# Performance work log

Hardware: AMD Instinct MI355X
Metric: run time of the kernel (lower is better)

The kernel has to match this reference:

```python
import jax, jax.numpy as jnp
import numpy as np

N_HEAD = 16

def setup_inputs() -> dict:
    key = jax.random.key(0)
    k1, k2, k3 = jax.random.split(key, 3)
    B, S, D = 4, 2048, 1024
    x = jax.random.normal(k1, (B, S, D), dtype=jnp.float32)
    w_attn = jax.random.normal(k2, (D, 3 * D), dtype=jnp.float32) * 0.02
    b_attn = jnp.zeros((3 * D,), dtype=jnp.float32)
    w_proj = jax.random.normal(k3, (D, D), dtype=jnp.float32) * 0.02
    b_proj = jnp.zeros((D,), dtype=jnp.float32)
    return {"x": x, "w_attn": w_attn, "b_attn": b_attn, "w_proj": w_proj, "b_proj": b_proj}

def reference(x, w_attn, b_attn, w_proj, b_proj):
    B, S, D = x.shape
    H = N_HEAD
    dh = D // H
    # c_attn (fan_in_fan_out Conv1D-style: y = x @ W + b)
    qkv = x @ w_attn + b_attn                      # [B,S,3D]
    q, k, v = jnp.split(qkv, 3, axis=-1)
    q = q.reshape(B, S, H, dh).transpose(0, 2, 1, 3)   # [B,H,S,dh]
    k = k.reshape(B, S, H, dh).transpose(0, 2, 3, 1)   # [B,H,dh,S]  (split_heads k=True)
    v = v.reshape(B, S, H, dh).transpose(0, 2, 1, 3)   # [B,H,S,dh]
    # scores = Q K^T, scaled by sqrt(d_head) since scale=True
    w = jnp.einsum('bhid,bhdj->bhij', q, k) / jnp.sqrt(jnp.asarray(dh, x.dtype))
    # causal mask blending exactly as original: w*b - 1e10*(1-b)
    b = jnp.tril(jnp.ones((S, S), dtype=x.dtype))[None, None]
    w = w * b - 1e10 * (1.0 - b)
    w = jax.nn.softmax(w, axis=-1)
    a = jnp.einsum('bhij,bhjd->bhid', w, v)        # [B,H,S,dh]
    a = a.transpose(0, 2, 1, 3).reshape(B, S, D)   # merge_heads
    out = a @ w_proj + b_proj                      # c_proj
    present = jnp.stack((k.transpose(0, 1, 3, 2), v))  # [2,B,H,S,dh]
    return out, present
```

## Files before the change

kernel.cpp:

```cpp
#include <hip/hip_runtime.h>
#include <stdint.h>

typedef unsigned short u16;
typedef __attribute__((ext_vector_type(8))) __bf16 bf16x8;
typedef __attribute__((ext_vector_type(4))) __bf16 bf16x4v;
typedef __attribute__((ext_vector_type(4))) float f32x4;
typedef __attribute__((ext_vector_type(4))) unsigned short u16x4;
typedef __attribute__((ext_vector_type(8))) unsigned short u16x8;

#define MFMA16(a,b,c) __builtin_amdgcn_mfma_f32_16x16x32_bf16(a,b,c,0,0,0)

static __device__ __forceinline__ float fexp2(float x){
#if __has_builtin(__builtin_amdgcn_exp2f)
  return __builtin_amdgcn_exp2f(x);
#else
  float r; asm("v_exp_f32 %0, %1" : "=v"(r) : "v"(x)); return r;
#endif
}

static __device__ __forceinline__ u16 f2b(float f){
  uint32_t u = __float_as_uint(f);
  u += 0x7fffu + ((u >> 16) & 1u);
  return (u16)(u >> 16);
}

static __device__ __forceinline__ void gload_lds16(const void* g, void* l){
  __builtin_amdgcn_global_load_lds(
      (__attribute__((address_space(1))) void*)(uintptr_t)g,
      (__attribute__((address_space(3))) void*)(uintptr_t)l,
      16, 0, 0);
}

__global__ __launch_bounds__(256) void fused_prep(
    const float* __restrict__ x, const float* __restrict__ w_attn,
    const float* __restrict__ w_proj,
    u16* __restrict__ x_bf, u16* __restrict__ wA_T, u16* __restrict__ wP_T)
{
  const int bid = blockIdx.x;
  const int tid = threadIdx.x;
  if (bid < 2048){
    const int n = 4 * 2048 * 1024;
    const int stride = 2048 * 256 * 4;
    int i = (bid * 256 + tid) * 4;
#pragma unroll
    for (int k = 0; k < 4; ++k, i += stride){
      if (i < n){
        float4 v = *(const float4*)(x + i);
        u16x4 o;
        o.x = f2b(v.x); o.y = f2b(v.y); o.z = f2b(v.z); o.w = f2b(v.w);
        *(u16x4*)(x_bf + i) = o;
      }
    }
    return;
  }
  __shared__ float tile[32][33];
  const float* in;
  u16* out;
  int K, N, nb, kb;
  if (bid < 5120){
    const int idx = bid - 2048;
    in = w_attn; out = wA_T; K = 1024; N = 3072;
    nb = (idx % 96) * 32; kb = (idx / 96) * 32;
  } else {
    const int idx = bid - 5120;
    in = w_proj; out = wP_T; K = 1024; N = 1024;
    nb = (idx % 32) * 32; kb = (idx / 32) * 32;
  }
  const int tx = tid & 31, ty = tid >> 5;
#pragma unroll
  for (int i = 0; i < 32; i += 8)
    tile[ty + i][tx] = in[(size_t)(kb + ty + i) * N + nb + tx];
  __syncthreads();
#pragma unroll
  for (int i = 0; i < 32; i += 8)
    out[(size_t)(nb + ty + i) * K + kb + tx] = f2b(tile[tx][ty + i]);
}

template<int MODE>
__global__ __launch_bounds__(512, 2) void gemm_pipe(
    const u16* __restrict__ A, const u16* __restrict__ Bt,
    const float* __restrict__ bias, float* __restrict__ Cout,
    u16* __restrict__ q_bf, u16* __restrict__ k_bf, u16* __restrict__ vT_bf,
    int N, int K)
{
  extern __shared__ u16 smem[];
  const int nT = K >> 5;
  const int tid = threadIdx.x;
  const int w = tid >> 6, lane = tid & 63;
  const int l15 = lane & 15, lhi = lane >> 4;
  const int wr = w >> 1, wc = w & 1;
  const int mBase = blockIdx.y * 256, nBase = blockIdx.x * 128;

  const int r0 = tid >> 2;
  const int ch = (tid & 3) ^ ((r0 >> 1) & 3);
  const u16* Ag  = A  + (size_t)(mBase + r0) * K + ch * 8;
  const u16* Ag2 = Ag + (size_t)128 * K;
  const u16* Bg  = Bt + (size_t)(nBase + r0) * K + ch * 8;

  f32x4 acc[4][4];
#pragma unroll
  for (int i = 0; i < 4; ++i)
#pragma unroll
    for (int j = 0; j < 4; ++j) acc[i][j] = f32x4{0.f, 0.f, 0.f, 0.f};

  auto stage = [&](int kt){
    char* buf = (char*)smem + (kt % 3) * 24576;
    const int kb = kt << 5;
    gload_lds16(Ag  + kb, buf + tid * 16);
    gload_lds16(Ag2 + kb, buf + 8192 + tid * 16);
    gload_lds16(Bg  + kb, buf + 16384 + tid * 16);
  };

  stage(0); stage(1);

  for (int kt = 0; kt < nT; ++kt){
    if (kt == nT - 1) asm volatile("s_waitcnt vmcnt(0)" ::: "memory");
    else              asm volatile("s_waitcnt vmcnt(3)" ::: "memory");
    __builtin_amdgcn_s_barrier();
    if (kt + 2 < nT) stage(kt + 2);
    const char* Ab = (const char*)smem + (kt % 3) * 24576;
    const char* Bb = Ab + 16384;
#define LDT(base, row) (*(const bf16x8*)((base) + ((row) << 6) + ((lhi ^ (((row) >> 1) & 3)) << 4)))
    bf16x8 a0, a1, a2, a3, b0, b1, b2, b3;
    {
      const int ar = wr * 64 + l15;
      a0 = LDT(Ab, ar); a1 = LDT(Ab, ar + 16); a2 = LDT(Ab, ar + 32); a3 = LDT(Ab, ar + 48);
      const int br = wc * 64 + l15;
      b0 = LDT(Bb, br); b1 = LDT(Bb, br + 16); b2 = LDT(Bb, br + 32); b3 = LDT(Bb, br + 48);
    }
#undef LDT
    __builtin_amdgcn_s_setprio(1);
    acc[0][0] = MFMA16(a0, b0, acc[0][0]); acc[0][1] = MFMA16(a0, b1, acc[0][1]);
    acc[0][2] = MFMA16(a0, b2, acc[0][2]); acc[0][3] = MFMA16(a0, b3, acc[0][3]);
    acc[1][0] = MFMA16(a1, b0, acc[1][0]); acc[1][1] = MFMA16(a1, b1, acc[1][1]);
    acc[1][2] = MFMA16(a1, b2, acc[1][2]); acc[1][3] = MFMA16(a1, b3, acc[1][3]);
    acc[2][0] = MFMA16(a2, b0, acc[2][0]); acc[2][1] = MFMA16(a2, b1, acc[2][1]);
    acc[2][2] = MFMA16(a2, b2, acc[2][2]); acc[2][3] = MFMA16(a2, b3, acc[2][3]);
    acc[3][0] = MFMA16(a3, b0, acc[3][0]); acc[3][1] = MFMA16(a3, b1, acc[3][1]);
    acc[3][2] = MFMA16(a3, b2, acc[3][2]); acc[3][3] = MFMA16(a3, b3, acc[3][3]);
    __builtin_amdgcn_s_setprio(0);
  }

  if (MODE == 0){
#pragma unroll
    for (int ni = 0; ni < 4; ++ni){
      const int col = nBase + wc * 64 + ni * 16 + l15;
      const float bv = bias[col];
#pragma unroll
      for (int mi = 0; mi < 4; ++mi)
#pragma unroll
        for (int r = 0; r < 4; ++r){
          const int row = mBase + wr * 64 + mi * 16 + lhi * 4 + r;
          Cout[(size_t)row * N + col] = acc[mi][ni][r] + bv;
        }
    }
    return;
  }

  const int sec = nBase >> 10;
  const int nn0 = nBase & 1023;
  const int bb_ = mBase >> 11;
  const int s0  = mBase & 2047;

  if (sec == 2){
#pragma unroll
    for (int ni = 0; ni < 4; ++ni){
      const int c = wc * 64 + ni * 16 + l15;
      const int nn = nn0 + c;
      const int h = nn >> 6, d = nn & 63;
      const float bv = bias[nBase + c];
#pragma unroll
      for (int mi = 0; mi < 4; ++mi){
        const int sb = s0 + wr * 64 + mi * 16 + lhi * 4;
        u16x4 pk;
#pragma unroll
        for (int r = 0; r < 4; ++r){
          const float v = acc[mi][ni][r] + bv;
          pk[r] = f2b(v);
          Cout[16777216 + ((size_t)(bb_ * 16 + h) * 2048 + sb + r) * 64 + d] = v;
        }
        *(u16x4*)(vT_bf + ((size_t)(bb_ * 16 + h) * 64 + d) * 2048 + sb) = pk;
      }
    }
    return;
  }

  __syncthreads();
  const float qscl = (sec == 0) ? 0.1803368801111204f : 1.0f;
#pragma unroll
  for (int ni = 0; ni < 4; ++ni){
    const int c = wc * 64 + ni * 16 + l15;
    const float bv = bias[nBase + c];
#pragma unroll
    for (int mi = 0; mi < 4; ++mi)
#pragma unroll
      for (int r = 0; r < 4; ++r){
        const int rl = wr * 64 + mi * 16 + lhi * 4 + r;
        smem[rl * 128 + (c ^ ((rl & 7) << 3))] = f2b((acc[mi][ni][r] + bv) * qscl);
      }
  }
  if (sec == 1){
#pragma unroll
    for (int ni = 0; ni < 4; ++ni){
      const int c = wc * 64 + ni * 16 + l15;
      const int nn = nn0 + c;
      const int h = nn >> 6, d = nn & 63;
      const float bv = bias[nBase + c];
#pragma unroll
      for (int mi = 0; mi < 4; ++mi)
#pragma unroll
        for (int r = 0; r < 4; ++r){
          const int s = s0 + wr * 64 + mi * 16 + lhi * 4 + r;
          Cout[8388608 + ((size_t)(bb_ * 16 + h) * 2048 + s) * 64 + d] = acc[mi][ni][r] + bv;
        }
    }
  }
  __syncthreads();
  {
    const int row = tid >> 1, half = tid & 1;
    u16* base = (sec == 0 ? q_bf : k_bf);
#pragma unroll
    for (int i = 0; i < 8; ++i){
      const int c0 = half * 64 + i * 8;
      const int h = (nn0 >> 6) + (c0 >> 6);
      u16x8 vv = *(const u16x8*)&smem[row * 128 + (c0 ^ ((row & 7) << 3))];
      *(u16x8*)(base + ((size_t)(bb_ * 16 + h) * 2048 + s0 + row) * 64 + (c0 & 63)) = vv;
    }
  }
}

__global__ __launch_bounds__(256) void attn_kern(
    const u16* __restrict__ q_bf, const u16* __restrict__ k_bf,
    const u16* __restrict__ vT_bf, u16* __restrict__ a_bf)
{
  const int S = 2048;
  const int id = (int)blockIdx.x + 32 * (int)blockIdx.y;
  const int xcd = id & 7, j = id >> 3;
  const int bh = xcd + 8 * (j & 7);
  const int qt = 31 - (j >> 3);

  const int tid = threadIdx.x, w = tid >> 6, lane = tid & 63;
  const int l15 = lane & 15, lhi = lane >> 4;
  const u16* qp = q_bf + (size_t)bh * S * 64;
  const char* kbytes = (const char*)(k_bf + (size_t)bh * S * 64);
  const char* vbytes = (const char*)(vT_bf + (size_t)bh * 64 * S);
  const int b = bh >> 4, h = bh & 15;

  __shared__ u16 Kbuf[2][64 * 64];
  __shared__ u16 Vbuf[2][64 * 64];
  __shared__ u16 P_all[4][16 * 64];
  char* Pc = (char*)&P_all[w][0];
  const int swz = (l15 & 7) << 4;

  const int srow = tid >> 3;
  const int sch  = (tid & 7) ^ (srow & 7);

  const int qr0 = qt * 64 + w * 16;
  const int nStage = qt + 1;

  bf16x8 qf0 = *(const bf16x8*)&qp[(qr0 + l15) * 64 + lhi * 8];
  bf16x8 qf1 = *(const bf16x8*)&qp[(qr0 + l15) * 64 + 32 + lhi * 8];

  f32x4 o[4];
#pragma unroll
  for (int df = 0; df < 4; ++df) o[df] = f32x4{0.f,0.f,0.f,0.f};
  float lsum = 0.f;

  int cur = 0;
  gload_lds16(kbytes + (size_t)srow * 128 + sch * 16,        (char*)Kbuf[0] + w * 1024);
  gload_lds16(kbytes + (size_t)(srow + 32) * 128 + sch * 16, (char*)Kbuf[0] + 4096 + w * 1024);
  gload_lds16(vbytes + (size_t)srow * 4096 + sch * 16,        (char*)Vbuf[0] + w * 1024);
  gload_lds16(vbytes + (size_t)(srow + 32) * 4096 + sch * 16, (char*)Vbuf[0] + 4096 + w * 1024);
  __syncthreads();

  for (int it = 0; it < nStage; ++it){
    const int jb = it * 64;
    if (it + 1 < nStage){
      const char* kb2 = kbytes + (size_t)(jb + 64) * 128;
      const char* vb2 = vbytes + (size_t)(jb + 64) * 2;
      char* kd = (char*)Kbuf[cur ^ 1];
      char* vd = (char*)Vbuf[cur ^ 1];
      gload_lds16(kb2 + (size_t)srow * 128 + sch * 16,        kd + w * 1024);
      gload_lds16(kb2 + (size_t)(srow + 32) * 128 + sch * 16, kd + 4096 + w * 1024);
      gload_lds16(vb2 + (size_t)srow * 4096 + sch * 16,        vd + w * 1024);
      gload_lds16(vb2 + (size_t)(srow + 32) * 4096 + sch * 16, vd + 4096 + w * 1024);
    }
    {
      const char* Kc = (const char*)Kbuf[cur];
      const char* Vc = (const char*)Vbuf[cur];
      f32x4 s[4];
      __builtin_amdgcn_s_setprio(1);
#pragma unroll
      for (int nf = 0; nf < 4; ++nf){
        const bf16x8 kf0 = *(const bf16x8*)(Kc + (((nf * 16 + l15) * 128 + 0 * 64 + lhi * 16) ^ swz));
        const bf16x8 kf1 = *(const bf16x8*)(Kc + (((nf * 16 + l15) * 128 + 1 * 64 + lhi * 16) ^ swz));
        f32x4 z = {0.f, 0.f, 0.f, 0.f};
        z = MFMA16(kf0, qf0, z);
        z = MFMA16(kf1, qf1, z);
        s[nf] = z;
      }
      __builtin_amdgcn_s_setprio(0);
      bf16x8 vf[8];
#pragma unroll
      for (int kk = 0; kk < 2; ++kk)
#pragma unroll
        for (int df = 0; df < 4; ++df)
          vf[kk*4+df] = *(const bf16x8*)(Vc + (((df * 16 + l15) * 128 + kk * 64 + lhi * 16) ^ swz));
      if (it == nStage - 1){
        const int q = qr0 + l15;
#pragma unroll
        for (int nf = 0; nf < 4; ++nf)
#pragma unroll
          for (int r = 0; r < 4; ++r){
            const int kv = jb + nf * 16 + lhi * 4 + r;
            if (kv > q) s[nf][r] = -1e10f;
          }
      }
      float p[16];
#pragma unroll
      for (int nf = 0; nf < 4; ++nf)
#pragma unroll
        for (int r = 0; r < 4; ++r) p[nf*4+r] = fexp2(s[nf][r]);
      lsum += (((p[0]+p[1])+(p[2]+p[3])) + ((p[4]+p[5])+(p[6]+p[7])))
            + (((p[8]+p[9])+(p[10]+p[11])) + ((p[12]+p[13])+(p[14]+p[15])));
#pragma unroll
      for (int nf = 0; nf < 4; ++nf){
        bf16x4v pk;
#pragma unroll
        for (int r = 0; r < 4; ++r) pk[r] = (__bf16)p[nf*4+r];
        *(bf16x4v*)(Pc + ((l15 * 128 + nf * 32 + lhi * 8) ^ swz)) = pk;
      }
      __builtin_amdgcn_s_setprio(1);
#pragma unroll
      for (int kk = 0; kk < 2; ++kk){
        const bf16x8 pa = *(const bf16x8*)(Pc + ((l15 * 128 + kk * 64 + lhi * 16) ^ swz));
#pragma unroll
        for (int df = 0; df < 4; ++df)
          o[df] = MFMA16(pa, vf[kk*4+df], o[df]);
      }
      __builtin_amdgcn_s_setprio(0);
    }
    __syncthreads();
    cur ^= 1;
  }

  {
    float rs = lsum;
    rs += __shfl_xor(rs, 16);
    rs += __shfl_xor(rs, 32);
    const float linv = 1.0f / rs;
    float lr[4];
#pragma unroll
    for (int r = 0; r < 4; ++r)
      lr[r] = __shfl(linv, (lane & 48) | (lhi * 4 + r));
#pragma unroll
    for (int r = 0; r < 4; ++r){
      const int qrow = qr0 + lhi * 4 + r;
#pragma unroll
      for (int df = 0; df < 4; ++df)
        a_bf[((size_t)b * 2048 + qrow) * 1024 + h * 64 + df * 16 + l15] = f2b(o[df][r] * lr[r]);
    }
  }
}

extern "C" void kernel_launch(void* const* d_in, const int* in_sizes, int n_in,
                              void* d_out, int out_size, void* d_ws, size_t ws_size,
                              hipStream_t stream)
{
  const float* x      = (const float*)d_in[0];
  const float* w_attn = (const float*)d_in[1];
  const float* b_attn = (const float*)d_in[2];
  const float* w_proj = (const float*)d_in[3];
  const float* b_proj = (const float*)d_in[4];
  float* out = (float*)d_out;
  char* ws = (char*)d_ws;
  const size_t MB = 1u << 20;
  u16* x_bf  = (u16*)(ws + 0);
  u16* wA_T  = (u16*)(ws + 16 * MB);
  u16* wP_T  = (u16*)(ws + 22 * MB);
  u16* q_bf  = (u16*)(ws + 24 * MB);
  u16* k_bf  = (u16*)(ws + 40 * MB);
  u16* vT_bf = (u16*)(ws + 56 * MB);
  u16* a_bf  = x_bf;

  fused_prep<<<dim3(6144), dim3(256), 0, stream>>>(x, w_attn, w_proj, x_bf, wA_T, wP_T);
  gemm_pipe<1><<<dim3(24, 32), dim3(512), 73728, stream>>>(
      x_bf, wA_T, b_attn, out, q_bf, k_bf, vT_bf, 3072, 1024);
  attn_kern<<<dim3(32, 64), dim3(256), 0, stream>>>(q_bf, k_bf, vT_bf, a_bf);
  gemm_pipe<0><<<dim3(8, 32), dim3(512), 73728, stream>>>(
      a_bf, wP_T, b_proj, out, nullptr, nullptr, nullptr, 1024, 1024);
}
```

Before: 172.7 us.

## Halve GEMM block to 4 waves, each computing 128x64 tile

```diff
diff --git a/kernel.cpp b/kernel.cpp
--- a/kernel.cpp
+++ b/kernel.cpp
@@ -77,7 +77,7 @@
 }
 
 template<int MODE>
-__global__ __launch_bounds__(512, 2) void gemm_pipe(
+__global__ __launch_bounds__(256, 2) void gemm_pipe(
     const u16* __restrict__ A, const u16* __restrict__ Bt,
     const float* __restrict__ bias, float* __restrict__ Cout,
     u16* __restrict__ q_bf, u16* __restrict__ k_bf, u16* __restrict__ vT_bf,
@@ -91,44 +91,48 @@
   const int wr = w >> 1, wc = w & 1;
   const int mBase = blockIdx.y * 256, nBase = blockIdx.x * 128;
 
-  const int r0 = tid >> 2;
-  const int ch = (tid & 3) ^ ((r0 >> 1) & 3);
-  const u16* Ag  = A  + (size_t)(mBase + r0) * K + ch * 8;
-  const u16* Ag2 = Ag + (size_t)128 * K;
-  const u16* Bg  = Bt + (size_t)(nBase + r0) * K + ch * 8;
-
-  f32x4 acc[4][4];
-#pragma unroll
-  for (int i = 0; i < 4; ++i)
+  const int qrow = lane >> 2;
+  const int ch = (lane & 3) ^ ((qrow >> 1) & 3);
+  const u16* AgB = A  + (size_t)(mBase + qrow) * K + ch * 8;
+  const u16* BgB = Bt + (size_t)(nBase + qrow) * K + ch * 8;
+  const int ln16 = lane << 4;
+
+  f32x4 acc[8][4];
+#pragma unroll
+  for (int i = 0; i < 8; ++i)
 #pragma unroll
     for (int j = 0; j < 4; ++j) acc[i][j] = f32x4{0.f, 0.f, 0.f, 0.f};
 
   auto stage = [&](int kt){
     char* buf = (char*)smem + (kt % 3) * 24576;
     const int kb = kt << 5;
-    gload_lds16(Ag  + kb, buf + tid * 16);
-    gload_lds16(Ag2 + kb, buf + 8192 + tid * 16);
-    gload_lds16(Bg  + kb, buf + 16384 + tid * 16);
+#pragma unroll
+    for (int i = 0; i < 4; ++i)
+      gload_lds16(AgB + (size_t)((w * 4 + i) * 16) * K + kb,
+                  buf + (w * 4 + i) * 1024 + ln16);
+#pragma unroll
+    for (int j = 0; j < 2; ++j)
+      gload_lds16(BgB + (size_t)((w * 2 + j) * 16) * K + kb,
+                  buf + 16384 + (w * 2 + j) * 1024 + ln16);
   };
 
   stage(0); stage(1);
 
   for (int kt = 0; kt < nT; ++kt){
     if (kt == nT - 1) asm volatile("s_waitcnt vmcnt(0)" ::: "memory");
-    else              asm volatile("s_waitcnt vmcnt(3)" ::: "memory");
+    else              asm volatile("s_waitcnt vmcnt(6)" ::: "memory");
     __builtin_amdgcn_s_barrier();
     if (kt + 2 < nT) stage(kt + 2);
     const char* Ab = (const char*)smem + (kt % 3) * 24576;
     const char* Bb = Ab + 16384;
 #define LDT(base, row) (*(const bf16x8*)((base) + ((row) << 6) + ((lhi ^ (((row) >> 1) & 3)) << 4)))
-    bf16x8 a0, a1, a2, a3, b0, b1, b2, b3;
+    bf16x8 b0, b1, b2, b3, a0, a1, a2, a3;
     {
-      const int ar = wr * 64 + l15;
-      a0 = LDT(Ab, ar); a1 = LDT(Ab, ar + 16); a2 = LDT(Ab, ar + 32); a3 = LDT(Ab, ar + 48);
       const int br = wc * 64 + l15;
       b0 = LDT(Bb, br); b1 = LDT(Bb, br + 16); b2 = LDT(Bb, br + 32); b3 = LDT(Bb, br + 48);
-    }
-#undef LDT
+      const int ar = wr * 128 + l15;
+      a0 = LDT(Ab, ar); a1 = LDT(Ab, ar + 16); a2 = LDT(Ab, ar + 32); a3 = LDT(Ab, ar + 48);
+    }
     __builtin_amdgcn_s_setprio(1);
     acc[0][0] = MFMA16(a0, b0, acc[0][0]); acc[0][1] = MFMA16(a0, b1, acc[0][1]);
     acc[0][2] = MFMA16(a0, b2, acc[0][2]); acc[0][3] = MFMA16(a0, b3, acc[0][3]);
@@ -139,6 +143,21 @@
     acc[3][0] = MFMA16(a3, b0, acc[3][0]); acc[3][1] = MFMA16(a3, b1, acc[3][1]);
     acc[3][2] = MFMA16(a3, b2, acc[3][2]); acc[3][3] = MFMA16(a3, b3, acc[3][3]);
     __builtin_amdgcn_s_setprio(0);
+    {
+      const int ar = wr * 128 + 64 + l15;
+      a0 = LDT(Ab, ar); a1 = LDT(Ab, ar + 16); a2 = LDT(Ab, ar + 32); a3 = LDT(Ab, ar + 48);
+    }
+#undef LDT
+    __builtin_amdgcn_s_setprio(1);
+    acc[4][0] = MFMA16(a0, b0, acc[4][0]); acc[4][1] = MFMA16(a0, b1, acc[4][1]);
+    acc[4][2] = MFMA16(a0, b2, acc[4][2]); acc[4][3] = MFMA16(a0, b3, acc[4][3]);
+    acc[5][0] = MFMA16(a1, b0, acc[5][0]); acc[5][1] = MFMA16(a1, b1, acc[5][1]);
+    acc[5][2] = MFMA16(a1, b2, acc[5][2]); acc[5][3] = MFMA16(a1, b3, acc[5][3]);
+    acc[6][0] = MFMA16(a2, b0, acc[6][0]); acc[6][1] = MFMA16(a2, b1, acc[6][1]);
+    acc[6][2] = MFMA16(a2, b2, acc[6][2]); acc[6][3] = MFMA16(a2, b3, acc[6][3]);
+    acc[7][0] = MFMA16(a3, b0, acc[7][0]); acc[7][1] = MFMA16(a3, b1, acc[7][1]);
+    acc[7][2] = MFMA16(a3, b2, acc[7][2]); acc[7][3] = MFMA16(a3, b3, acc[7][3]);
+    __builtin_amdgcn_s_setprio(0);
   }
 
   if (MODE == 0){
@@ -147,10 +166,10 @@
       const int col = nBase + wc * 64 + ni * 16 + l15;
       const float bv = bias[col];
 #pragma unroll
-      for (int mi = 0; mi < 4; ++mi)
+      for (int mi = 0; mi < 8; ++mi)
 #pragma unroll
         for (int r = 0; r < 4; ++r){
-          const int row = mBase + wr * 64 + mi * 16 + lhi * 4 + r;
+          const int row = mBase + wr * 128 + mi * 16 + lhi * 4 + r;
           Cout[(size_t)row * N + col] = acc[mi][ni][r] + bv;
         }
     }
@@ -170,8 +189,8 @@
       const int h = nn >> 6, d = nn & 63;
       const float bv = bias[nBase + c];
 #pragma unroll
-      for (int mi = 0; mi < 4; ++mi){
-        const int sb = s0 + wr * 64 + mi * 16 + lhi * 4;
+      for (int mi = 0; mi < 8; ++mi){
+        const int sb = s0 + wr * 128 + mi * 16 + lhi * 4;
         u16x4 pk;
 #pragma unroll
         for (int r = 0; r < 4; ++r){
@@ -192,10 +211,10 @@
     const int c = wc * 64 + ni * 16 + l15;
     const float bv = bias[nBase + c];
 #pragma unroll
-    for (int mi = 0; mi < 4; ++mi)
+    for (int mi = 0; mi < 8; ++mi)
 #pragma unroll
       for (int r = 0; r < 4; ++r){
-        const int rl = wr * 64 + mi * 16 + lhi * 4 + r;
+        const int rl = wr * 128 + mi * 16 + lhi * 4 + r;
         smem[rl * 128 + (c ^ ((rl & 7) << 3))] = f2b((acc[mi][ni][r] + bv) * qscl);
       }
   }
@@ -207,21 +226,21 @@
       const int h = nn >> 6, d = nn & 63;
       const float bv = bias[nBase + c];
 #pragma unroll
-      for (int mi = 0; mi < 4; ++mi)
+      for (int mi = 0; mi < 8; ++mi)
 #pragma unroll
         for (int r = 0; r < 4; ++r){
-          const int s = s0 + wr * 64 + mi * 16 + lhi * 4 + r;
+          const int s = s0 + wr * 128 + mi * 16 + lhi * 4 + r;
           Cout[8388608 + ((size_t)(bb_ * 16 + h) * 2048 + s) * 64 + d] = acc[mi][ni][r] + bv;
         }
     }
   }
   __syncthreads();
   {
-    const int row = tid >> 1, half = tid & 1;
+    const int row = tid;
     u16* base = (sec == 0 ? q_bf : k_bf);
 #pragma unroll
-    for (int i = 0; i < 8; ++i){
-      const int c0 = half * 64 + i * 8;
+    for (int i = 0; i < 16; ++i){
+      const int c0 = i * 8;
       const int h = (nn0 >> 6) + (c0 >> 6);
       u16x8 vv = *(const u16x8*)&smem[row * 128 + (c0 ^ ((row & 7) << 3))];
       *(u16x8*)(base + ((size_t)(bb_ * 16 + h) * 2048 + s0 + row) * 64 + (c0 & 63)) = vv;
@@ -384,9 +403,9 @@
   u16* a_bf  = x_bf;
 
   fused_prep<<<dim3(6144), dim3(256), 0, stream>>>(x, w_attn, w_proj, x_bf, wA_T, wP_T);
-  gemm_pipe<1><<<dim3(24, 32), dim3(512), 73728, stream>>>(
+  gemm_pipe<1><<<dim3(24, 32), dim3(256), 73728, stream>>>(
       x_bf, wA_T, b_attn, out, q_bf, k_bf, vT_bf, 3072, 1024);
   attn_kern<<<dim3(32, 64), dim3(256), 0, stream>>>(q_bf, k_bf, vT_bf, a_bf);
-  gemm_pipe<0><<<dim3(8, 32), dim3(512), 73728, stream>>>(
+  gemm_pipe<0><<<dim3(8, 32), dim3(256), 73728, stream>>>(
       a_bf, wP_T, b_proj, out, nullptr, nullptr, nullptr, 1024, 1024);
 }
```

Result: no change. 170.4 us (-1.3%).
